# Kernel optimization log

Measured on AMD Instinct MI355X. Metric: run time of the kernel, lower is better.

Reference implementation:

```python
import math
import jax, jax.numpy as jnp
import numpy as np

B, N, D, H = 4, 2048, 512, 8
HD = D // H


def setup_inputs() -> dict:
    key = jax.random.key(0)
    ks = jax.random.split(key, 7)
    w_scale = 1.0 / math.sqrt(D)  # keep logits in a sane range (like default init)
    return {
        "q": jax.random.normal(ks[0], (B, N, D), dtype=jnp.float32),
        "mask": jax.random.randint(ks[1], (B, N), 0, 2) == 1,  # True = masked key
        "attn_bias": jax.random.normal(ks[2], (B, N, N), dtype=jnp.float32),
        "Wq": jax.random.normal(ks[3], (D, D), dtype=jnp.float32) * w_scale,
        "Wk": jax.random.normal(ks[4], (D, D), dtype=jnp.float32) * w_scale,
        "Wv": jax.random.normal(ks[5], (D, D), dtype=jnp.float32) * w_scale,
        "Wo": jax.random.normal(ks[6], (D, D), dtype=jnp.float32) * w_scale,
    }


def _heads(v):
    # [B, N, D] -> [H, B, N, HD]  (mirrors reshape + movedim(-2, 0))
    b, n, d = v.shape
    return v.reshape(b, n, H, HD).transpose(2, 0, 1, 3)


def reference(q, mask, attn_bias, Wq, Wk, Wv, Wo):
    # Linear projections (torch Linear: x @ W.T)
    qh = _heads(q @ Wq.T)
    kh = _heads(q @ Wk.T)   # self-attention: h defaults to q
    vh = _heads(q @ Wv.T)
    # scores: [H, B, Nq, Nk]
    scores = jnp.einsum("hbqd,hbkd->hbqk", qh, kh) / math.sqrt(HD)
    scores = scores + attn_bias[None]                     # broadcast over heads
    scores = jnp.where(mask[None, :, None, :], -jnp.inf, scores)
    attn = jax.nn.softmax(scores, axis=-1)
    out = jnp.einsum("hbqk,hbkd->hbqd", attn, vh)         # [H, B, Nq, HD]
    out = out.transpose(1, 2, 0, 3).reshape(q.shape[0], q.shape[1], D)
    return out @ Wo.T
```

## Files before the change

### kernel.cpp

```cpp
#include <hip/hip_runtime.h>
#include <stdint.h>


typedef __attribute__((ext_vector_type(8))) short short8;
typedef __attribute__((ext_vector_type(4))) short short4v;
typedef __attribute__((ext_vector_type(4))) float f32x4;

#define DEV static __device__ __forceinline__

constexpr int Bc = 4, Nc = 2048, Dc = 512, Hc = 8, HDc = 64;
constexpr int Mc = Bc * Nc;
constexpr int QKVNc = 3 * Dc;
constexpr float L2E = 1.44269504f;

DEV short bf16cast(float f) {
  return (short)__builtin_bit_cast(unsigned short, (__bf16)f);
}
DEV unsigned cvt_pk_bf16(float a, float b) {
  unsigned short lb = __builtin_bit_cast(unsigned short, (__bf16)a);
  unsigned short hb = __builtin_bit_cast(unsigned short, (__bf16)b);
  return (unsigned)lb | ((unsigned)hb << 16);
}
DEV unsigned pack_shorts(short a, short b) {
  return (unsigned)(unsigned short)a | ((unsigned)(unsigned short)b << 16);
}
DEV short8 cvt8(float4 a, float4 b) {
  union { short8 s; uint4 u; } r;
  r.u.x = cvt_pk_bf16(a.x, a.y); r.u.y = cvt_pk_bf16(a.z, a.w);
  r.u.z = cvt_pk_bf16(b.x, b.y); r.u.w = cvt_pk_bf16(b.z, b.w);
  return r.s;
}
DEV float fast_exp2(float x) {
#if __has_builtin(__builtin_amdgcn_exp2f)
  return __builtin_amdgcn_exp2f(x);
#else
  return exp2f(x);
#endif
}
DEV void permswap32(unsigned& a, unsigned& b) {
  asm volatile("v_permlane32_swap_b32 %0, %1" : "+v"(a), "+v"(b));
}
DEV void gl_lds16(const short* g, short* l) {
  __builtin_amdgcn_global_load_lds(
      (const __attribute__((address_space(1))) void*)g,
      (__attribute__((address_space(3))) void*)l, 16, 0, 0);
}

template<bool A_F32, int BN, bool OUT_F32>
__global__ __launch_bounds__(256, 2) void gemm_bt(const void* __restrict__ Av,
                                                  const float* __restrict__ B0,
                                                  const float* __restrict__ B1,
                                                  const float* __restrict__ B2,
                                                  void* __restrict__ Cv,
                                                  int M, int N,
                                                  int qcols, float cscale) {
  constexpr int K = 512;
  constexpr int BG = BN / 32;
  constexpr int MT = (BN == 128) ? 4 : 2;
  constexpr int NT = 4;
  __shared__ __align__(16) short At[128 * 72];
  __shared__ __align__(16) short Bt[BN * 72];
  const int tid = threadIdx.x, lane = tid & 63, wv = tid >> 6;
  const int quad = lane >> 4, l16 = lane & 15;
  const int mbase = blockIdx.y * 128, nbase = blockIdx.x * BN;
  const int wr = (BN == 128) ? (wv >> 1) * 64 : wv * 32;
  const int wc = (BN == 128) ? (wv & 1) * 64 : 0;
  const float* Bsel = nbase < 512 ? B0 : (nbase < 1024 ? B1 : B2);
  const int col0 = nbase & 511;
  const float scale = (nbase < qcols) ? cscale : 1.0f;
  f32x4 acc[MT][NT] = {};
  float4 apf[4][2]; short8 aph[4];
  float4 bpf[BG][2];
#pragma unroll
  for (int i = 0; i < 4; i++) {
    int flat = i * 256 + tid, row = flat >> 3, ch8 = (flat & 7) * 8;
    if (A_F32) {
      const float* Af = (const float*)Av;
      apf[i][0] = *(const float4*)&Af[(size_t)(mbase + row) * K + ch8];
      apf[i][1] = *(const float4*)&Af[(size_t)(mbase + row) * K + ch8 + 4];
    } else {
      aph[i] = *(const short8*)&((const short*)Av)[(size_t)(mbase + row) * K + ch8];
    }
  }
#pragma unroll
  for (int i = 0; i < BG; i++) {
    int flat = i * 256 + tid, row = flat >> 3, ch8 = (flat & 7) * 8;
    bpf[i][0] = *(const float4*)&Bsel[(size_t)(col0 + row) * K + ch8];
    bpf[i][1] = *(const float4*)&Bsel[(size_t)(col0 + row) * K + ch8 + 4];
  }
  for (int k0 = 0; k0 < K; k0 += 64) {
    __syncthreads();
#pragma unroll
    for (int i = 0; i < 4; i++) {
      int flat = i * 256 + tid, row = flat >> 3, ch8 = (flat & 7) * 8;
      *(short8*)&At[row * 72 + ch8] = A_F32 ? cvt8(apf[i][0], apf[i][1]) : aph[i];
    }
#pragma unroll
    for (int i = 0; i < BG; i++) {
      int flat = i * 256 + tid, row = flat >> 3, ch8 = (flat & 7) * 8;
      *(short8*)&Bt[row * 72 + ch8] = cvt8(bpf[i][0], bpf[i][1]);
    }
    if (k0 + 64 < K) {
#pragma unroll
      for (int i = 0; i < 4; i++) {
        int flat = i * 256 + tid, row = flat >> 3, ch8 = (flat & 7) * 8;
        if (A_F32) {
          const float* Af = (const float*)Av;
          apf[i][0] = *(const float4*)&Af[(size_t)(mbase + row) * K + k0 + 64 + ch8];
          apf[i][1] = *(const float4*)&Af[(size_t)(mbase + row) * K + k0 + 64 + ch8 + 4];
        } else {
          aph[i] = *(const short8*)&((const short*)Av)[(size_t)(mbase + row) * K + k0 + 64 + ch8];
        }
      }
#pragma unroll
      for (int i = 0; i < BG; i++) {
        int flat = i * 256 + tid, row = flat >> 3, ch8 = (flat & 7) * 8;
        bpf[i][0] = *(const float4*)&Bsel[(size_t)(col0 + row) * K + k0 + 64 + ch8];
        bpf[i][1] = *(const float4*)&Bsel[(size_t)(col0 + row) * K + k0 + 64 + ch8 + 4];
      }
    }
    __syncthreads();
#pragma unroll
    for (int s = 0; s < 2; s++) {
      short8 af[MT], bf[NT];
#pragma unroll
      for (int t = 0; t < MT; t++)
        af[t] = *(short8*)&At[(wr + t * 16 + l16) * 72 + quad * 8 + s * 32];
#pragma unroll
      for (int t = 0; t < NT; t++)
        bf[t] = *(short8*)&Bt[(wc + t * 16 + l16) * 72 + quad * 8 + s * 32];
#pragma unroll
      for (int mt = 0; mt < MT; mt++)
#pragma unroll
        for (int nt = 0; nt < NT; nt++)
          acc[mt][nt] = __builtin_amdgcn_mfma_f32_16x16x32_bf16(af[mt], bf[nt], acc[mt][nt], 0, 0, 0);
    }
  }
#pragma unroll
  for (int mt = 0; mt < MT; mt++)
#pragma unroll
    for (int nt = 0; nt < NT; nt++)
#pragma unroll
      for (int r = 0; r < 4; r++) {
        int row = mbase + wr + mt * 16 + quad * 4 + r;
        int col = nbase + wc + nt * 16 + l16;
        float v = acc[mt][nt][r] * scale;
        if (OUT_F32) ((float*)Cv)[(size_t)row * N + col] = v;
        else         ((short*)Cv)[(size_t)row * N + col] = bf16cast(v);
      }
}

__global__ __launch_bounds__(256, 2) void attn_kernel(const short* __restrict__ QKV,
                                                      const float* __restrict__ bias,
                                                      const void* __restrict__ mask,
                                                      short* __restrict__ Aout) {
  __shared__ __align__(16) short Kt[2][64 * 64];
  __shared__ __align__(16) short Vt[2][64 * 64];
  __shared__ __align__(16) float mlds[Nc];
  __shared__ int mflag;
  const int tid = threadIdx.x, lane = tid & 63, wv = tid >> 6;
  const int quad = lane >> 4, l16 = lane & 15;
  const int qt = blockIdx.x & 15, h = (blockIdx.x >> 4) & 7, b = (int)(blockIdx.x >> 7);
  const int qrow0 = qt * 128;
  const int q0 = qrow0 + wv * 32 + l16;
  const float* biasq0 = bias + ((size_t)b * Nc + q0) * Nc;
  const float* biasq1 = biasq0 + (size_t)16 * Nc;
  const short* Kbase = QKV + Dc + h * HDc;
  const short* Vbase = QKV + 2 * Dc + h * HDc;

#pragma unroll
  for (int j = 0; j < 2; j++) {
    int seg = wv * 2 + j, c = seg * 64 + lane;
    int row = c >> 3, ch = c & 7;
    gl_lds16(&Kbase[(size_t)(b * Nc + row) * QKVNc + ((ch ^ (row & 7)) << 3)],
             &Kt[0][seg * 512]);
  }

  short8 qf[2][2];
  {
    const short* qp0 = QKV + (size_t)(b * Nc + q0) * QKVNc + h * HDc + quad * 8;
    qf[0][0] = *(const short8*)qp0;
    qf[0][1] = *(const short8*)(qp0 + 32);
    const short* qp1 = qp0 + (size_t)16 * QKVNc;
    qf[1][0] = *(const short8*)qp1;
    qf[1][1] = *(const short8*)(qp1 + 32);
  }

  const int vp = tid & 31, vq = tid >> 5;
  const int vperm = (vp & 25) | ((vp & 4) >> 1) | ((vp & 2) << 1);
  const int vwbase = (((vperm >> 2)) << 3) + 2 * (vperm & 3);

  short8 v0pre, v1pre;
  v0pre = *(const short8*)&Vbase[(size_t)(b * Nc + 2 * vp) * QKVNc + vq * 8];
  v1pre = *(const short8*)&Vbase[(size_t)(b * Nc + 2 * vp + 1) * QKVNc + vq * 8];
  float4 bpre[2][4];
#pragma unroll
  for (int t = 0; t < 4; t++) {
    bpre[0][t] = *(const float4*)&biasq0[t * 16 + quad * 4];
    bpre[1][t] = *(const float4*)&biasq1[t * 16 + quad * 4];
  }

  if (tid == 0) mflag = 0;
  __syncthreads();
  {
    const uchar4* mw = (const uchar4*)((const char*)mask + (size_t)b * 2048);
    int acc = 0;
#pragma unroll
    for (int i = tid; i < 512; i += 256) {
      uchar4 v = mw[i];
      acc |= (int)v.y | (int)v.z | (int)v.w;
    }
    if (acc) atomicOr(&mflag, 1);
  }
  __syncthreads();
  {
    int isbyte = mflag;
    const unsigned char* mb = (const unsigned char*)mask + (size_t)b * 2048;
    const int* mi = (const int*)mask + (size_t)b * 2048;
    for (int i = tid; i < Nc; i += 256) {
      int v = isbyte ? (int)mb[i] : mi[i];
      mlds[i] = v ? -1e30f : 0.0f;
    }
  }

  const short ONEB = (short)0x3F80;
  const short8 ones = { ONEB, ONEB, ONEB, ONEB, ONEB, ONEB, ONEB, ONEB };

  f32x4 oacc[2][4] = {};
  f32x4 sumacc[2] = {};

  for (int kt = 0; kt < 32; kt++) {
    const int cur = kt & 1, nxt = cur ^ 1;
    const int kb = kt * 64;
    const int kbn = ((kt + 1) & 31) * 64;

#pragma unroll
    for (int j = 0; j < 8; j++) {
      int hd = vq * 8 + j;
      *(unsigned*)&Vt[cur][hd * 64 + (vwbase ^ ((hd & 7) << 3))] =
          pack_shorts(v0pre[j], v1pre[j]);
    }
    __syncthreads();

#pragma unroll
    for (int j = 0; j < 2; j++) {
      int seg = wv * 2 + j, c = seg * 64 + lane;
      int row = c >> 3, ch = c & 7;
      gl_lds16(&Kbase[(size_t)(b * Nc + kbn + row) * QKVNc + ((ch ^ (row & 7)) << 3)],
               &Kt[nxt][seg * 512]);
    }
    v0pre = *(const short8*)&Vbase[(size_t)(b * Nc + kbn + 2 * vp) * QKVNc + vq * 8];
    v1pre = *(const short8*)&Vbase[(size_t)(b * Nc + kbn + 2 * vp + 1) * QKVNc + vq * 8];

    f32x4 sacc[2][4];
#pragma unroll
    for (int t = 0; t < 4; t++) {
      float4 mv = *(const float4*)&mlds[kb + t * 16 + quad * 4];
      sacc[0][t][0] = mv.x; sacc[0][t][1] = mv.y; sacc[0][t][2] = mv.z; sacc[0][t][3] = mv.w;
      sacc[1][t] = sacc[0][t];
    }

    __builtin_amdgcn_s_setprio(1);
#pragma unroll
    for (int s = 0; s < 2; s++)
#pragma unroll
      for (int t = 0; t < 4; t++) {
        short8 kf = *(short8*)&Kt[cur][(t * 16 + l16) * 64 + (((quad + 4 * s) ^ (l16 & 7)) << 3)];
        sacc[0][t] = __builtin_amdgcn_mfma_f32_16x16x32_bf16(kf, qf[0][s], sacc[0][t], 0, 0, 0);
        sacc[1][t] = __builtin_amdgcn_mfma_f32_16x16x32_bf16(kf, qf[1][s], sacc[1][t], 0, 0, 0);
      }
    __builtin_amdgcn_s_setprio(0);

    short8 pf[2][2];
#pragma unroll
    for (int n = 0; n < 2; n++) {
      unsigned pw[4][2];
#pragma unroll
      for (int t = 0; t < 4; t++) {
        float p0 = fast_exp2(__builtin_fmaf(bpre[n][t].x, L2E, sacc[n][t][0]));
        float p1 = fast_exp2(__builtin_fmaf(bpre[n][t].y, L2E, sacc[n][t][1]));
        float p2 = fast_exp2(__builtin_fmaf(bpre[n][t].z, L2E, sacc[n][t][2]));
        float p3 = fast_exp2(__builtin_fmaf(bpre[n][t].w, L2E, sacc[n][t][3]));
        pw[t][0] = cvt_pk_bf16(p0, p1);
        pw[t][1] = cvt_pk_bf16(p2, p3);
      }
      permswap32(pw[0][0], pw[1][0]); permswap32(pw[0][1], pw[1][1]);
      permswap32(pw[2][0], pw[3][0]); permswap32(pw[2][1], pw[3][1]);
      union { unsigned u[4]; short8 s; }
          a0{{pw[0][0], pw[0][1], pw[1][0], pw[1][1]}},
          a1{{pw[2][0], pw[2][1], pw[3][0], pw[3][1]}};
      pf[n][0] = a0.s; pf[n][1] = a1.s;
    }

#pragma unroll
    for (int t = 0; t < 4; t++) {
      bpre[0][t] = *(const float4*)&biasq0[kbn + t * 16 + quad * 4];
      bpre[1][t] = *(const float4*)&biasq1[kbn + t * 16 + quad * 4];
    }

    __builtin_amdgcn_s_setprio(1);
#pragma unroll
    for (int s = 0; s < 2; s++) {
      sumacc[0] = __builtin_amdgcn_mfma_f32_16x16x32_bf16(pf[0][s], ones, sumacc[0], 0, 0, 0);
      sumacc[1] = __builtin_amdgcn_mfma_f32_16x16x32_bf16(pf[1][s], ones, sumacc[1], 0, 0, 0);
#pragma unroll
      for (int t = 0; t < 4; t++) {
        short8 vf = *(short8*)&Vt[cur][(t * 16 + l16) * 64 + (((quad + 4 * s) ^ (l16 & 7)) << 3)];
        oacc[0][t] = __builtin_amdgcn_mfma_f32_16x16x32_bf16(pf[0][s], vf, oacc[0][t], 0, 0, 0);
        oacc[1][t] = __builtin_amdgcn_mfma_f32_16x16x32_bf16(pf[1][s], vf, oacc[1][t], 0, 0, 0);
      }
    }
    __builtin_amdgcn_s_setprio(0);
  }

#pragma unroll
  for (int m = 0; m < 2; m++)
#pragma unroll
    for (int r = 0; r < 4; r++) {
      float inv = 1.0f / sumacc[m][r];
      int row = b * Nc + qrow0 + wv * 32 + m * 16 + quad * 4 + r;
#pragma unroll
      for (int t = 0; t < 4; t++)
        Aout[(size_t)row * Dc + h * HDc + t * 16 + l16] = bf16cast(oacc[m][t][r] * inv);
    }
}

extern "C" void kernel_launch(void* const* d_in, const int* in_sizes, int n_in,
                              void* d_out, int out_size, void* d_ws, size_t ws_size,
                              hipStream_t stream) {
  const float* q    = (const float*)d_in[0];
  const void*  mask = d_in[1];
  const float* bias = (const float*)d_in[2];
  const float* Wq   = (const float*)d_in[3];
  const float* Wk   = (const float*)d_in[4];
  const float* Wv   = (const float*)d_in[5];
  const float* Wo   = (const float*)d_in[6];
  float* out = (float*)d_out;

  char* ws = (char*)d_ws;
  short* QKV  = (short*)ws;  ws += (size_t)Mc * QKVNc * 2;
  short* aout = (short*)ws;  ws += (size_t)Mc * Dc * 2;

  gemm_bt<true, 128, false><<<dim3(QKVNc / 128, Mc / 128), dim3(256), 0, stream>>>(
      (const void*)q, Wq, Wk, Wv, (void*)QKV, Mc, QKVNc, Dc, 0.125f * L2E);
  attn_kernel<<<dim3(Bc * Hc * 16), dim3(256), 0, stream>>>(QKV, bias, mask, aout);
  gemm_bt<false, 64, true><<<dim3(Dc / 64, Mc / 128), dim3(256), 0, stream>>>(
      (const void*)aout, Wo, Wo, Wo, (void*)out, Mc, Dc, 0, 1.0f);
}
```

Before: 256.4 us.

## Process two key tiles per barrier with four-stage K/V LDS buffering

The attention loop now handles two 64-key tiles per iteration, using four K/V shared-memory buffers so each barrier covers 128 keys and prefetches the next pair. This halves the number of __syncthreads and gives more time to hide global/LDS latency. In exchange, LDS use doubles (from about 40KB to 72KB per block) and register pressure rises from doubled V and bias prefetch registers. Both could hurt occupancy under the launch bound of two blocks per CU.

```diff
diff --git a/kernel.cpp b/kernel.cpp
--- a/kernel.cpp
+++ b/kernel.cpp
@@ -154,8 +154,8 @@
                                                       const float* __restrict__ bias,
                                                       const void* __restrict__ mask,
                                                       short* __restrict__ Aout) {
-  __shared__ __align__(16) short Kt[2][64 * 64];
-  __shared__ __align__(16) short Vt[2][64 * 64];
+  __shared__ __align__(16) short Kt[4][64 * 64];
+  __shared__ __align__(16) short Vt[4][64 * 64];
   __shared__ __align__(16) float mlds[Nc];
   __shared__ int mflag;
   const int tid = threadIdx.x, lane = tid & 63, wv = tid >> 6;
@@ -169,12 +169,14 @@
   const short* Vbase = QKV + 2 * Dc + h * HDc;
 
 #pragma unroll
-  for (int j = 0; j < 2; j++) {
-    int seg = wv * 2 + j, c = seg * 64 + lane;
-    int row = c >> 3, ch = c & 7;
-    gl_lds16(&Kbase[(size_t)(b * Nc + row) * QKVNc + ((ch ^ (row & 7)) << 3)],
-             &Kt[0][seg * 512]);
-  }
+  for (int j = 0; j < 2; j++)
+#pragma unroll
+    for (int g = 0; g < 2; g++) {
+      int seg = wv * 2 + g, c = seg * 64 + lane;
+      int row = c >> 3, ch = c & 7;
+      gl_lds16(&Kbase[(size_t)(b * Nc + j * 64 + row) * QKVNc + ((ch ^ (row & 7)) << 3)],
+               &Kt[j][seg * 512]);
+    }
 
   short8 qf[2][2];
   {
@@ -190,14 +192,17 @@
   const int vperm = (vp & 25) | ((vp & 4) >> 1) | ((vp & 2) << 1);
   const int vwbase = (((vperm >> 2)) << 3) + 2 * (vperm & 3);
 
-  short8 v0pre, v1pre;
-  v0pre = *(const short8*)&Vbase[(size_t)(b * Nc + 2 * vp) * QKVNc + vq * 8];
-  v1pre = *(const short8*)&Vbase[(size_t)(b * Nc + 2 * vp + 1) * QKVNc + vq * 8];
-  float4 bpre[2][4];
-#pragma unroll
-  for (int t = 0; t < 4; t++) {
-    bpre[0][t] = *(const float4*)&biasq0[t * 16 + quad * 4];
-    bpre[1][t] = *(const float4*)&biasq1[t * 16 + quad * 4];
+  short8 v0pre[2], v1pre[2];
+  float4 bpre[2][2][4];
+#pragma unroll
+  for (int j = 0; j < 2; j++) {
+    v0pre[j] = *(const short8*)&Vbase[(size_t)(b * Nc + j * 64 + 2 * vp) * QKVNc + vq * 8];
+    v1pre[j] = *(const short8*)&Vbase[(size_t)(b * Nc + j * 64 + 2 * vp + 1) * QKVNc + vq * 8];
+#pragma unroll
+    for (int t = 0; t < 4; t++) {
+      bpre[j][0][t] = *(const float4*)&biasq0[j * 64 + t * 16 + quad * 4];
+      bpre[j][1][t] = *(const float4*)&biasq1[j * 64 + t * 16 + quad * 4];
+    }
   }
 
   if (tid == 0) mflag = 0;
@@ -229,88 +234,99 @@
   f32x4 oacc[2][4] = {};
   f32x4 sumacc[2] = {};
 
-  for (int kt = 0; kt < 32; kt++) {
-    const int cur = kt & 1, nxt = cur ^ 1;
-    const int kb = kt * 64;
-    const int kbn = ((kt + 1) & 31) * 64;
-
-#pragma unroll
-    for (int j = 0; j < 8; j++) {
-      int hd = vq * 8 + j;
-      *(unsigned*)&Vt[cur][hd * 64 + (vwbase ^ ((hd & 7) << 3))] =
-          pack_shorts(v0pre[j], v1pre[j]);
-    }
+  for (int pd = 0; pd < 16; pd++) {
+    const int pb = (pd & 1) * 2;
+    const int nb = 2 - pb;
+
+#pragma unroll
+    for (int j = 0; j < 2; j++)
+#pragma unroll
+      for (int jj = 0; jj < 8; jj++) {
+        int hd = vq * 8 + jj;
+        *(unsigned*)&Vt[pb + j][hd * 64 + (vwbase ^ ((hd & 7) << 3))] =
+            pack_shorts(v0pre[j][jj], v1pre[j][jj]);
+      }
     __syncthreads();
 
 #pragma unroll
     for (int j = 0; j < 2; j++) {
-      int seg = wv * 2 + j, c = seg * 64 + lane;
-      int row = c >> 3, ch = c & 7;
-      gl_lds16(&Kbase[(size_t)(b * Nc + kbn + row) * QKVNc + ((ch ^ (row & 7)) << 3)],
-               &Kt[nxt][seg * 512]);
-    }
-    v0pre = *(const short8*)&Vbase[(size_t)(b * Nc + kbn + 2 * vp) * QKVNc + vq * 8];
-    v1pre = *(const short8*)&Vbase[(size_t)(b * Nc + kbn + 2 * vp + 1) * QKVNc + vq * 8];
-
-    f32x4 sacc[2][4];
-#pragma unroll
-    for (int t = 0; t < 4; t++) {
-      float4 mv = *(const float4*)&mlds[kb + t * 16 + quad * 4];
-      sacc[0][t][0] = mv.x; sacc[0][t][1] = mv.y; sacc[0][t][2] = mv.z; sacc[0][t][3] = mv.w;
-      sacc[1][t] = sacc[0][t];
-    }
-
-    __builtin_amdgcn_s_setprio(1);
-#pragma unroll
-    for (int s = 0; s < 2; s++)
+      const int kn = ((2 * pd + 2 + j) & 31) * 64;
+#pragma unroll
+      for (int g = 0; g < 2; g++) {
+        int seg = wv * 2 + g, c = seg * 64 + lane;
+        int row = c >> 3, ch = c & 7;
+        gl_lds16(&Kbase[(size_t)(b * Nc + kn + row) * QKVNc + ((ch ^ (row & 7)) << 3)],
+                 &Kt[nb + j][seg * 512]);
+      }
+      v0pre[j] = *(const short8*)&Vbase[(size_t)(b * Nc + kn + 2 * vp) * QKVNc + vq * 8];
+      v1pre[j] = *(const short8*)&Vbase[(size_t)(b * Nc + kn + 2 * vp + 1) * QKVNc + vq * 8];
+    }
+
+#pragma unroll
+    for (int j = 0; j < 2; j++) {
+      const int kb = (2 * pd + j) * 64;
+      const int knb = ((2 * pd + j + 2) & 31) * 64;
+
+      f32x4 sacc[2][4];
 #pragma unroll
       for (int t = 0; t < 4; t++) {
-        short8 kf = *(short8*)&Kt[cur][(t * 16 + l16) * 64 + (((quad + 4 * s) ^ (l16 & 7)) << 3)];
-        sacc[0][t] = __builtin_amdgcn_mfma_f32_16x16x32_bf16(kf, qf[0][s], sacc[0][t], 0, 0, 0);
-        sacc[1][t] = __builtin_amdgcn_mfma_f32_16x16x32_bf16(kf, qf[1][s], sacc[1][t], 0, 0, 0);
-      }
-    __builtin_amdgcn_s_setprio(0);
-
-    short8 pf[2][2];
-#pragma unroll
-    for (int n = 0; n < 2; n++) {
-      unsigned pw[4][2];
+        float4 mv = *(const float4*)&mlds[kb + t * 16 + quad * 4];
+        sacc[0][t][0] = mv.x; sacc[0][t][1] = mv.y; sacc[0][t][2] = mv.z; sacc[0][t][3] = mv.w;
+        sacc[1][t] = sacc[0][t];
+      }
+
+      __builtin_amdgcn_s_setprio(1);
+#pragma unroll
+      for (int s = 0; s < 2; s++)
+#pragma unroll
+        for (int t = 0; t < 4; t++) {
+          short8 kf = *(short8*)&Kt[pb + j][(t * 16 + l16) * 64 + (((quad + 4 * s) ^ (l16 & 7)) << 3)];
+          sacc[0][t] = __builtin_amdgcn_mfma_f32_16x16x32_bf16(kf, qf[0][s], sacc[0][t], 0, 0, 0);
+          sacc[1][t] = __builtin_amdgcn_mfma_f32_16x16x32_bf16(kf, qf[1][s], sacc[1][t], 0, 0, 0);
+        }
+      __builtin_amdgcn_s_setprio(0);
+
+      short8 pf[2][2];
+#pragma unroll
+      for (int n = 0; n < 2; n++) {
+        unsigned pw[4][2];
+#pragma unroll
+        for (int t = 0; t < 4; t++) {
+          float p0 = fast_exp2(__builtin_fmaf(bpre[j][n][t].x, L2E, sacc[n][t][0]));
+          float p1 = fast_exp2(__builtin_fmaf(bpre[j][n][t].y, L2E, sacc[n][t][1]));
+          float p2 = fast_exp2(__builtin_fmaf(bpre[j][n][t].z, L2E, sacc[n][t][2]));
+          float p3 = fast_exp2(__builtin_fmaf(bpre[j][n][t].w, L2E, sacc[n][t][3]));
+          pw[t][0] = cvt_pk_bf16(p0, p1);
+          pw[t][1] = cvt_pk_bf16(p2, p3);
+        }
+        permswap32(pw[0][0], pw[1][0]); permswap32(pw[0][1], pw[1][1]);
+        permswap32(pw[2][0], pw[3][0]); permswap32(pw[2][1], pw[3][1]);
+        union { unsigned u[4]; short8 s; }
+            a0{{pw[0][0], pw[0][1], pw[1][0], pw[1][1]}},
+            a1{{pw[2][0], pw[2][1], pw[3][0], pw[3][1]}};
+        pf[n][0] = a0.s; pf[n][1] = a1.s;
+      }
+
 #pragma unroll
       for (int t = 0; t < 4; t++) {
-        float p0 = fast_exp2(__builtin_fmaf(bpre[n][t].x, L2E, sacc[n][t][0]));
-        float p1 = fast_exp2(__builtin_fmaf(bpre[n][t].y, L2E, sacc[n][t][1]));
-        float p2 = fast_exp2(__builtin_fmaf(bpre[n][t].z, L2E, sacc[n][t][2]));
-        float p3 = fast_exp2(__builtin_fmaf(bpre[n][t].w, L2E, sacc[n][t][3]));
-        pw[t][0] = cvt_pk_bf16(p0, p1);
-        pw[t][1] = cvt_pk_bf16(p2, p3);
-      }
-      permswap32(pw[0][0], pw[1][0]); permswap32(pw[0][1], pw[1][1]);
-      permswap32(pw[2][0], pw[3][0]); permswap32(pw[2][1], pw[3][1]);
-      union { unsigned u[4]; short8 s; }
-          a0{{pw[0][0], pw[0][1], pw[1][0], pw[1][1]}},
-          a1{{pw[2][0], pw[2][1], pw[3][0], pw[3][1]}};
-      pf[n][0] = a0.s; pf[n][1] = a1.s;
-    }
-
-#pragma unroll
-    for (int t = 0; t < 4; t++) {
-      bpre[0][t] = *(const float4*)&biasq0[kbn + t * 16 + quad * 4];
-      bpre[1][t] = *(const float4*)&biasq1[kbn + t * 16 + quad * 4];
-    }
-
-    __builtin_amdgcn_s_setprio(1);
-#pragma unroll
-    for (int s = 0; s < 2; s++) {
-      sumacc[0] = __builtin_amdgcn_mfma_f32_16x16x32_bf16(pf[0][s], ones, sumacc[0], 0, 0, 0);
-      sumacc[1] = __builtin_amdgcn_mfma_f32_16x16x32_bf16(pf[1][s], ones, sumacc[1], 0, 0, 0);
-#pragma unroll
-      for (int t = 0; t < 4; t++) {
-        short8 vf = *(short8*)&Vt[cur][(t * 16 + l16) * 64 + (((quad + 4 * s) ^ (l16 & 7)) << 3)];
-        oacc[0][t] = __builtin_amdgcn_mfma_f32_16x16x32_bf16(pf[0][s], vf, oacc[0][t], 0, 0, 0);
-        oacc[1][t] = __builtin_amdgcn_mfma_f32_16x16x32_bf16(pf[1][s], vf, oacc[1][t], 0, 0, 0);
-      }
-    }
-    __builtin_amdgcn_s_setprio(0);
+        bpre[j][0][t] = *(const float4*)&biasq0[knb + t * 16 + quad * 4];
+        bpre[j][1][t] = *(const float4*)&biasq1[knb + t * 16 + quad * 4];
+      }
+
+      __builtin_amdgcn_s_setprio(1);
+#pragma unroll
+      for (int s = 0; s < 2; s++) {
+        sumacc[0] = __builtin_amdgcn_mfma_f32_16x16x32_bf16(pf[0][s], ones, sumacc[0], 0, 0, 0);
+        sumacc[1] = __builtin_amdgcn_mfma_f32_16x16x32_bf16(pf[1][s], ones, sumacc[1], 0, 0, 0);
+#pragma unroll
+        for (int t = 0; t < 4; t++) {
+          short8 vf = *(short8*)&Vt[pb + j][(t * 16 + l16) * 64 + (((quad + 4 * s) ^ (l16 & 7)) << 3)];
+          oacc[0][t] = __builtin_amdgcn_mfma_f32_16x16x32_bf16(pf[0][s], vf, oacc[0][t], 0, 0, 0);
+          oacc[1][t] = __builtin_amdgcn_mfma_f32_16x16x32_bf16(pf[1][s], vf, oacc[1][t], 0, 0, 0);
+        }
+      }
+      __builtin_amdgcn_s_setprio(0);
+    }
   }
 
 #pragma unroll
```

New measurement: 248.2 us. -3.2%, faster.
